# Optimization experiments

Measured on AMD Instinct MI355X. Metric: run time of the kernel, lower is better.

## Reference

```python
import jax, jax.numpy as jnp
import numpy as np

N, C, D = 8192, 21, 5


def setup_inputs() -> dict:
    key = jax.random.key(0)
    k1, k2 = jax.random.split(key)
    U = jax.random.normal(k1, (N, C), dtype=jnp.float32)
    ref = jax.random.normal(k2, (N, D), dtype=jnp.float32)
    return {"U": U, "ref": ref}


def reference(U, ref):
    # Exact Gaussian lattice filter: out_i = sum_j exp(-||f_i - f_j||^2 / 2) U_j - U_i
    # (the permutohedral lattice is an approximation of this kernel matvec).
    sq = jnp.sum(ref * ref, axis=-1)                      # [N]
    # pairwise squared distances: ||f_i||^2 + ||f_j||^2 - 2 f_i.f_j
    d2 = sq[:, None] + sq[None, :] - 2.0 * (ref @ ref.T)  # [N, N]
    W = jnp.exp(-0.5 * jnp.maximum(d2, 0.0))              # [N, N] Gaussian kernel
    return W @ U - U                                      # (W - I) @ U
```

## Files before the change

kernel.cpp:

```cpp
#include <hip/hip_runtime.h>


#define NN 8192
#define CC 21
#define DD 5
#define NTILE_G (NN / 32)
#define ROWS 32
#define NIB (NN / ROWS)
#define JSPLIT 2
#define TPB (NTILE_G / JSPLIT)
#define MAINT 1024
#define NWAVE 16
#define TPW (TPB / NWAVE)

#define F_OFF 0
#define U_OFF (NTILE_G * 64 * 16)

typedef __attribute__((ext_vector_type(2)))  __fp16   fp16x2;
typedef __attribute__((ext_vector_type(8)))  _Float16 f16x8;
typedef __attribute__((ext_vector_type(16))) float    f32x16;
typedef __attribute__((ext_vector_type(4)))  unsigned u32x4;

__global__ __launch_bounds__(256)
void pack_frags(const float* __restrict__ U, const float* __restrict__ ref,
                char* __restrict__ ws) {
    const float NH = -0.7213475204444817f;
    const int q = blockIdx.x * 256 + threadIdx.x;
    if (q < NTILE_G * 64) {
        const int tile = q >> 6, ln = q & 63;
        const int j = tile * 32 + (ln & 31);
        const float* fj = ref + (size_t)j * DD;
        _Float16 h_[5], l_[5];
        float sq = 0.f;
        #pragma unroll
        for (int d = 0; d < DD; ++d) {
            const float f = fj[d];
            sq = fmaf(f, f, sq);
            h_[d] = (_Float16)f;
            l_[d] = (_Float16)(f - (float)h_[d]);
        }
        const _Float16 aj = (_Float16)(NH * sq);
        _Float16 v[8] __attribute__((aligned(16)));
        if (ln < 32) {
            v[0]=h_[0]; v[1]=h_[1]; v[2]=h_[2]; v[3]=h_[3];
            v[4]=h_[4]; v[5]=l_[0]; v[6]=l_[1]; v[7]=l_[2];
        } else {
            v[0]=l_[3]; v[1]=l_[4]; v[2]=h_[0]; v[3]=h_[1];
            v[4]=h_[2]; v[5]=h_[3]; v[6]=h_[4]; v[7]=aj;
        }
        u32x4 pk; __builtin_memcpy(&pk, v, 16);
        *(u32x4*)(ws + F_OFF + (size_t)q * 16) = pk;
    } else {
        const int qu = q - NTILE_G * 64;
        const int ln = qu & 63, kt = (qu >> 6) & 1, tile = qu >> 7;
        const int c = ln & 31, g = ln >> 5;
        _Float16 v[8] __attribute__((aligned(16))) = {0,0,0,0,0,0,0,0};
        if (c < CC) {
            #pragma unroll
            for (int e = 0; e < 8; ++e) {
                const int j = tile * 32 + kt * 16 + (e & 3) + 8 * (e >> 2) + 4 * g;
                v[e] = (_Float16)U[(size_t)j * CC + c];
            }
        }
        u32x4 pk; __builtin_memcpy(&pk, v, 16);
        *(u32x4*)(ws + U_OFF + (size_t)qu * 16) = pk;
    }
}

__global__ __launch_bounds__(MAINT, 8)
void lattice_main(const float* __restrict__ U, const float* __restrict__ ref,
                  const char* __restrict__ ws, float* __restrict__ out) {
    __shared__ __align__(16) float red[NWAVE * ROWS * 32];

    const int t    = threadIdx.x;
    const int lane = t & 63;
    const int wv   = t >> 6;
    const int h    = lane >> 5;
    const int m    = lane & 31;
    const int ibase = blockIdx.x * ROWS;
    const int jc    = blockIdx.y;
    const float L  = 1.4426950408889634f;
    const float NH = -0.7213475204444817f;

    const float* fiP = ref + (size_t)(ibase + m) * DD;
    const float fi0 = fiP[0], fi1 = fiP[1], fi2 = fiP[2], fi3 = fiP[3], fi4 = fiP[4];
    const float ai = NH * (fi0*fi0 + fi1*fi1 + fi2*fi2 + fi3*fi3 + fi4*fi4);
    f16x8 bfi;
    {
        const float sf[5] = {L*fi0, L*fi1, L*fi2, L*fi3, L*fi4};
        _Float16 hi_[5], lo_[5];
        #pragma unroll
        for (int d = 0; d < DD; ++d) {
            hi_[d] = (_Float16)sf[d];
            lo_[d] = (_Float16)(sf[d] - (float)hi_[d]);
        }
        _Float16 bv[8] __attribute__((aligned(16)));
        bv[0] = h ? hi_[3] : hi_[0];
        bv[1] = h ? hi_[4] : hi_[1];
        bv[2] = h ? lo_[0] : hi_[2];
        bv[3] = h ? lo_[1] : hi_[3];
        bv[4] = h ? lo_[2] : hi_[4];
        bv[5] = h ? lo_[3] : hi_[0];
        bv[6] = h ? lo_[4] : hi_[1];
        bv[7] = h ? (_Float16)1.0f : hi_[2];
        __builtin_memcpy(&bfi, bv, 16);
    }

    f32x16 acc;
    #pragma unroll
    for (int r = 0; r < 16; ++r) acc[r] = 0.f;

    const char* Fws = ws + F_OFF;
    const char* Uws = ws + U_OFF;
    const int tile0 = jc * TPB + wv * TPW;

    for (int s = 0; s < TPW; ++s) {
        const int tile = tile0 + s;
        const u32x4 fr = *(const u32x4*)(Fws + ((size_t)(tile * 64 + lane)) * 16);
        const u32x4 b0 = *(const u32x4*)(Uws + ((size_t)((tile * 2 + 0) * 64 + lane)) * 16);
        const u32x4 b1 = *(const u32x4*)(Uws + ((size_t)((tile * 2 + 1) * 64 + lane)) * 16);

        f32x16 sacc;
        #pragma unroll
        for (int r = 0; r < 16; ++r) sacc[r] = 0.f;
        sacc = __builtin_amdgcn_mfma_f32_32x32x16_f16(
            __builtin_bit_cast(f16x8, fr), bfi, sacc, 0, 0, 0);

        float e[16];
        #pragma unroll
        for (int r = 0; r < 16; ++r)
            e[r] = __builtin_amdgcn_exp2f(ai + sacc[r]);

        fp16x2 p[8];
        #pragma unroll
        for (int k = 0; k < 8; ++k)
            p[k] = __builtin_amdgcn_cvt_pkrtz(e[2*k], e[2*k+1]);
        f16x8 a0, a1;
        __builtin_memcpy(&a0, &p[0], 16);
        __builtin_memcpy(&a1, &p[4], 16);

        acc = __builtin_amdgcn_mfma_f32_32x32x16_f16(
            a0, __builtin_bit_cast(f16x8, b0), acc, 0, 0, 0);
        acc = __builtin_amdgcn_mfma_f32_32x32x16_f16(
            a1, __builtin_bit_cast(f16x8, b1), acc, 0, 0, 0);
    }

    #pragma unroll
    for (int r = 0; r < 16; ++r) {
        const int row = (r & 3) + 8 * (r >> 2) + 4 * h;
        red[wv * (ROWS * 32) + row * 32 + m] = acc[r];
    }
    __syncthreads();

    {
        const int row = t >> 5, col = t & 31;
        float s = 0.f;
        #pragma unroll
        for (int w = 0; w < NWAVE; ++w) s += red[w * (ROWS * 32) + row * 32 + col];
        if (col < CC) {
            const size_t o = (size_t)(ibase + row) * CC + col;
            if (jc == 0) s -= U[o];
            unsafeAtomicAdd(&out[o], s);
        }
    }
}

extern "C" void kernel_launch(void* const* d_in, const int* in_sizes, int n_in,
                              void* d_out, int out_size, void* d_ws, size_t ws_size,
                              hipStream_t stream) {
    const float* U   = (const float*)d_in[0];
    const float* ref = (const float*)d_in[1];
    float* out = (float*)d_out;
    char* ws = (char*)d_ws;

    (void)hipMemsetAsync(out, 0, (size_t)out_size * sizeof(float), stream);

    const int pack_threads = NTILE_G * 64 + NTILE_G * 2 * 64;
    pack_frags<<<pack_threads / 256, 256, 0, stream>>>(U, ref, ws);

    dim3 grid(NIB, JSPLIT);
    lattice_main<<<grid, MAINT, 0, stream>>>(U, ref, (const char*)ws, out);
}
```

Measured before the change: 24.89 us.

## Replace memset and atomic adds with per-split partial buffers plus combine kernel

The memset of the output and the atomic accumulation across the two j-splits are removed. Each split now writes its partial sums to its own workspace buffer, and a small combine kernel adds the two partials and subtracts U with vectorized loads and stores. The row bias ai is also folded into the MFMA accumulator init, which saves one add per exp. The cost is an extra kernel launch and an extra pass over the partial buffers in place of the memset launch and the atomics.

```diff
diff --git a/kernel.cpp b/kernel.cpp
--- a/kernel.cpp
+++ b/kernel.cpp
@@ -15,6 +15,8 @@
 
 #define F_OFF 0
 #define U_OFF (NTILE_G * 64 * 16)
+#define P_OFF (U_OFF + NTILE_G * 2 * 64 * 16)
+#define PSZ   (NN * CC * 4)
 
 typedef __attribute__((ext_vector_type(2)))  __fp16   fp16x2;
 typedef __attribute__((ext_vector_type(8)))  _Float16 f16x8;
@@ -69,7 +71,7 @@
 
 __global__ __launch_bounds__(MAINT, 8)
 void lattice_main(const float* __restrict__ U, const float* __restrict__ ref,
-                  const char* __restrict__ ws, float* __restrict__ out) {
+                  char* __restrict__ ws, float* __restrict__ out) {
     __shared__ __align__(16) float red[NWAVE * ROWS * 32];
 
     const int t    = threadIdx.x;
@@ -106,6 +108,10 @@
         __builtin_memcpy(&bfi, bv, 16);
     }
 
+    f32x16 cini;
+    #pragma unroll
+    for (int r = 0; r < 16; ++r) cini[r] = ai;
+
     f32x16 acc;
     #pragma unroll
     for (int r = 0; r < 16; ++r) acc[r] = 0.f;
@@ -120,16 +126,13 @@
         const u32x4 b0 = *(const u32x4*)(Uws + ((size_t)((tile * 2 + 0) * 64 + lane)) * 16);
         const u32x4 b1 = *(const u32x4*)(Uws + ((size_t)((tile * 2 + 1) * 64 + lane)) * 16);
 
-        f32x16 sacc;
-        #pragma unroll
-        for (int r = 0; r < 16; ++r) sacc[r] = 0.f;
-        sacc = __builtin_amdgcn_mfma_f32_32x32x16_f16(
-            __builtin_bit_cast(f16x8, fr), bfi, sacc, 0, 0, 0);
+        f32x16 sacc = __builtin_amdgcn_mfma_f32_32x32x16_f16(
+            __builtin_bit_cast(f16x8, fr), bfi, cini, 0, 0, 0);
 
         float e[16];
         #pragma unroll
         for (int r = 0; r < 16; ++r)
-            e[r] = __builtin_amdgcn_exp2f(ai + sacc[r]);
+            e[r] = __builtin_amdgcn_exp2f(sacc[r]);
 
         fp16x2 p[8];
         #pragma unroll
@@ -153,16 +156,31 @@
     __syncthreads();
 
     {
+        float* po = (float*)(ws + P_OFF + (size_t)jc * PSZ);
         const int row = t >> 5, col = t & 31;
         float s = 0.f;
         #pragma unroll
         for (int w = 0; w < NWAVE; ++w) s += red[w * (ROWS * 32) + row * 32 + col];
-        if (col < CC) {
-            const size_t o = (size_t)(ibase + row) * CC + col;
-            if (jc == 0) s -= U[o];
-            unsafeAtomicAdd(&out[o], s);
-        }
-    }
+        if (col < CC)
+            po[(size_t)(ibase + row) * CC + col] = s;
+    }
+}
+
+__global__ __launch_bounds__(256)
+void combine(const char* __restrict__ ws, const float* __restrict__ U,
+             float* __restrict__ out) {
+    const int i = blockIdx.x * 256 + threadIdx.x;
+    const float4* p0 = (const float4*)(ws + P_OFF);
+    const float4* p1 = (const float4*)(ws + P_OFF + PSZ);
+    const float4 a = p0[i];
+    const float4 b = p1[i];
+    const float4 u = ((const float4*)U)[i];
+    float4 o;
+    o.x = a.x + b.x - u.x;
+    o.y = a.y + b.y - u.y;
+    o.z = a.z + b.z - u.z;
+    o.w = a.w + b.w - u.w;
+    ((float4*)out)[i] = o;
 }
 
 extern "C" void kernel_launch(void* const* d_in, const int* in_sizes, int n_in,
@@ -173,11 +191,11 @@
     float* out = (float*)d_out;
     char* ws = (char*)d_ws;
 
-    (void)hipMemsetAsync(out, 0, (size_t)out_size * sizeof(float), stream);
-
     const int pack_threads = NTILE_G * 64 + NTILE_G * 2 * 64;
     pack_frags<<<pack_threads / 256, 256, 0, stream>>>(U, ref, ws);
 
     dim3 grid(NIB, JSPLIT);
-    lattice_main<<<grid, MAINT, 0, stream>>>(U, ref, (const char*)ws, out);
-}
+    lattice_main<<<grid, MAINT, 0, stream>>>(U, ref, ws, out);
+
+    combine<<<(NN * CC / 4) / 256, 256, 0, stream>>>(ws, U, out);
+}
```

After: 36.36 us. +46.1%, slower.
